# Performance work log

Measured on AMD Instinct MI355X. Metric: run time of the kernel, lower is better.

Reference implementation:

```python
import jax, jax.numpy as jnp
import numpy as np

N_COMPANY = 16384
N_SECTOR = 64
PER_SECTOR = N_COMPANY // N_SECTOR  # 256, companies grouped contiguously by sector
WIN = 32
D_IN = 16
H_GRU = 64
H_INTRA = 64
H_INTER = 64
D_OUT = 4
E_INNER = 524288  # avg degree 32 within sectors


def setup_inputs() -> dict:
    key = jax.random.key(0)
    ks = jax.random.split(key, 20)
    s = 0.05

    daily_data_batch = jax.random.normal(ks[0], (WIN, N_COMPANY, D_IN), jnp.float32)

    rng = np.random.default_rng(0)
    dst = rng.integers(0, N_COMPANY, E_INNER)
    src = (dst // PER_SECTOR) * PER_SECTOR + rng.integers(0, PER_SECTOR, E_INNER)  # same-sector neighbors
    inner_edge = jnp.asarray(np.stack([src, dst]), jnp.int32)

    a, b = np.meshgrid(np.arange(N_SECTOR), np.arange(N_SECTOR), indexing="ij")
    oe = np.stack([a.ravel(), b.ravel()])
    oe = oe[:, oe[0] != oe[1]]  # fully-connected sector graph w/o self loops (GAT adds them)
    outer_edge = jnp.asarray(oe, jnp.int32)

    sector_ids = jnp.asarray(np.arange(N_COMPANY) // PER_SECTOR, jnp.int32)

    inp = {
        "daily_data_batch": daily_data_batch,
        "inner_edge": inner_edge,
        "outer_edge": outer_edge,
        "sector_ids": sector_ids,
        # BatchNorm1d(input_dim*window_size)
        "bn_gamma": jnp.ones((D_IN * WIN,), jnp.float32),
        "bn_beta": jnp.zeros((D_IN * WIN,), jnp.float32),
        # Graph GRU (per-node learnable initial hidden state)
        "gru_Wih": s * jax.random.normal(ks[1], (D_IN, 3 * H_GRU), jnp.float32),
        "gru_Whh": s * jax.random.normal(ks[2], (H_GRU, 3 * H_GRU), jnp.float32),
        "gru_bih": jnp.zeros((3 * H_GRU,), jnp.float32),
        "gru_bhh": jnp.zeros((3 * H_GRU,), jnp.float32),
        "gru_h0": s * jax.random.normal(ks[3], (N_COMPANY, H_GRU), jnp.float32),
        # intra-sector GATConv
        "gat1_W": s * jax.random.normal(ks[4], (H_GRU, H_INTRA), jnp.float32),
        "gat1_asrc": s * jax.random.normal(ks[5], (H_INTRA,), jnp.float32),
        "gat1_adst": s * jax.random.normal(ks[6], (H_INTRA,), jnp.float32),
        "gat1_b": jnp.zeros((H_INTRA,), jnp.float32),
        # inter-sector GATConv
        "gat2_W": s * jax.random.normal(ks[7], (H_INTRA, H_INTER), jnp.float32),
        "gat2_asrc": s * jax.random.normal(ks[8], (H_INTER,), jnp.float32),
        "gat2_adst": s * jax.random.normal(ks[9], (H_INTER,), jnp.float32),
        "gat2_b": jnp.zeros((H_INTER,), jnp.float32),
        # fusion / logit heads
        "fusion_W": s * jax.random.normal(ks[10], (H_GRU + H_INTRA + H_INTER, H_GRU), jnp.float32),
        "fusion_b": jnp.zeros((H_GRU,), jnp.float32),
        "logit_W": s * jax.random.normal(ks[11], (H_GRU, D_OUT), jnp.float32),
        "logit_b": jnp.zeros((D_OUT,), jnp.float32),
    }
    return inp


def _gat(x, edge, W, a_src, a_dst, b):
    """PyG-style single-head GATConv with default add_self_loops=True."""
    N = x.shape[0]
    h = x @ W  # [N, F]
    loops = jnp.arange(N, dtype=edge.dtype)
    src = jnp.concatenate([edge[0], loops])
    dst = jnp.concatenate([edge[1], loops])
    e = jax.nn.leaky_relu(h[src] @ a_src + h[dst] @ a_dst, 0.2)  # [E]
    # segment softmax over incoming edges per dst node
    m = jax.ops.segment_max(e, dst, num_segments=N)
    ex = jnp.exp(e - m[dst])
    denom = jax.ops.segment_sum(ex, dst, num_segments=N)
    alpha = ex / (denom[dst] + 1e-16)
    out = jax.ops.segment_sum(h[src] * alpha[:, None], dst, num_segments=N)
    return out + b


def _forward(daily_data_batch, inner_edge, outer_edge, sector_ids,
             bn_gamma, bn_beta,
             gru_Wih, gru_Whh, gru_bih, gru_bhh, gru_h0,
             gat1_W, gat1_asrc, gat1_adst, gat1_b,
             gat2_W, gat2_asrc, gat2_adst, gat2_b,
             fusion_W, fusion_b, logit_W, logit_b):
    W, N, D = daily_data_batch.shape
    # BatchNorm1d over companies (train-mode batch stats, eps=1e-5)
    xb = jnp.transpose(daily_data_batch, (1, 0, 2)).reshape(N, W * D)
    mu = xb.mean(axis=0)
    var = xb.var(axis=0)
    xb = (xb - mu) * jax.lax.rsqrt(var + 1e-5) * bn_gamma + bn_beta
    x = jnp.transpose(xb.reshape(N, W, D), (1, 0, 2))  # [W, N, D]

    # GRU over the window, per-node hidden state
    def step(h, xt):
        gi = xt @ gru_Wih + gru_bih
        gh = h @ gru_Whh + gru_bhh
        ir, iz, inn = jnp.split(gi, 3, axis=-1)
        hr, hz, hn = jnp.split(gh, 3, axis=-1)
        r = jax.nn.sigmoid(ir + hr)
        z = jax.nn.sigmoid(iz + hz)
        n = jnp.tanh(inn + r * hn)
        return (1.0 - z) * n + z * h, None

    seq_emb, _ = jax.lax.scan(step, gru_h0, x)  # [N, H_GRU]

    intra_emb = _gat(seq_emb, inner_edge, gat1_W, gat1_asrc, gat1_adst, gat1_b)  # [N, H_INTRA]

    # sector_separater + per-sector max pooling == segment_max
    sec_pool = jax.ops.segment_max(intra_emb, sector_ids, num_segments=N_SECTOR)  # [S, H_INTRA]
    sec_emb = _gat(sec_pool, outer_edge, gat2_W, gat2_asrc, gat2_adst, gat2_b)  # [S, H_INTER]
    sec_broad = sec_emb[sector_ids]  # repeat_interleave back to companies

    fusion_vec = jnp.concatenate([seq_emb, sec_broad, intra_emb], axis=-1)
    fusion_vec = jax.nn.relu(fusion_vec @ fusion_W + fusion_b)
    logits = jax.nn.softmax(fusion_vec @ logit_W + logit_b, axis=1)
    logits = jnp.cumsum(logits, axis=1)
    eps = 5e-08
    return jnp.clip(logits, eps, 1.0 - eps)


def reference(daily_data_batch, inner_edge, outer_edge, sector_ids,
              bn_gamma, bn_beta,
              gru_Wih, gru_Whh, gru_bih, gru_bhh, gru_h0,
              gat1_W, gat1_asrc, gat1_adst, gat1_b,
              gat2_W, gat2_asrc, gat2_adst, gat2_b,
              fusion_W, fusion_b, logit_W, logit_b):
    return _forward(daily_data_batch, inner_edge, outer_edge, sector_ids,
                    bn_gamma, bn_beta,
                    gru_Wih, gru_Whh, gru_bih, gru_bhh, gru_h0,
                    gat1_W, gat1_asrc, gat1_adst, gat1_b,
                    gat2_W, gat2_asrc, gat2_adst, gat2_b,
                    fusion_W, fusion_b, logit_W, logit_b)
```

## Files before the change

### kernel.cpp

```cpp
#include <hip/hip_runtime.h>

#define NC 16384
#define WIN 32
#define DI 16
#define EI 524288

typedef unsigned short u16;
typedef unsigned char u8;
typedef unsigned int u32;
typedef __attribute__((ext_vector_type(8))) short bfrag8;
typedef __attribute__((ext_vector_type(4))) float facc4;

__device__ __forceinline__ float bf2f(u16 u) { return __uint_as_float(((u32)u) << 16); }
__device__ __forceinline__ u16 f2bf(float f) {
    u32 u = __float_as_uint(f);
    u += 0x7FFFu + ((u >> 16) & 1u);
    return (u16)(u >> 16);
}
__device__ __forceinline__ float frcp(float x) { return __builtin_amdgcn_rcpf(x); }
__device__ __forceinline__ float lrelu(float x) { return x >= 0.0f ? x : 0.2f * x; }
__device__ __forceinline__ float loadf(const void* p, size_t i, bool f32) {
    return f32 ? ((const float*)p)[i] : bf2f(((const u16*)p)[i]);
}
__device__ __forceinline__ bool is_f32(const void* gamma) {
    return ((const u32*)gamma)[0] == 0x3F800000u;
}

#define O_SCALE 0
#define O_SHIFT 512
#define O_WIH   1024
#define O_WHH   4096
#define O_BIH   16384
#define O_BHH   16576
#define O_G1W   16768
#define O_G1AS  20864
#define O_G1AD  20928
#define O_G1B   20992
#define O_G2W   21056
#define O_G2AS  25152
#define O_G2AD  25216
#define O_G2B   25280
#define O_FB    25344
#define O_LW    25408
#define O_LB    25664
#define O_FW16  25668
#define O_BNACC 31812
#define O_SEQ   40960
#define O_H1    1089536
#define O_INTRA 1613824
#define O_SPOOL 2138112
#define O_AS    2158592
#define O_AD    2174976
#define O_M     2191360

__global__ __launch_bounds__(256) void k_convert(const void* __restrict__ gamma,
                                                 const void* __restrict__ wih,
                                                 const void* __restrict__ whh,
                                                 const void* __restrict__ bih,
                                                 const void* __restrict__ bhh,
                                                 const void* __restrict__ g1w,
                                                 const void* __restrict__ g1as,
                                                 const void* __restrict__ g1ad,
                                                 const void* __restrict__ g1b,
                                                 const void* __restrict__ g2w,
                                                 const void* __restrict__ g2as,
                                                 const void* __restrict__ g2ad,
                                                 const void* __restrict__ g2b,
                                                 const void* __restrict__ fw,
                                                 const void* __restrict__ fb,
                                                 const void* __restrict__ lw,
                                                 const void* __restrict__ lb,
                                                 float* __restrict__ ws,
                                                 uint4* __restrict__ M16) {
    int gt = blockIdx.x * 256 + threadIdx.x;
    const int GS = 64 * 256;
    bool f32 = is_f32(gamma);
    u16* fw16 = (u16*)(ws + O_FW16);
    for (int i = gt; i < 3072; i += GS) ws[O_WIH + i] = loadf(wih, i, f32);
    for (int i = gt; i < 12288; i += GS) {
        ws[O_WHH + i] = loadf(whh, i, f32);
        fw16[i] = f32 ? f2bf(((const float*)fw)[i]) : ((const u16*)fw)[i];
    }
    for (int i = gt; i < 192; i += GS) {
        ws[O_BIH + i] = loadf(bih, i, f32);
        ws[O_BHH + i] = loadf(bhh, i, f32);
    }
    for (int i = gt; i < 4096; i += GS) {
        ws[O_G1W + i] = loadf(g1w, i, f32);
        ws[O_G2W + i] = loadf(g2w, i, f32);
    }
    if (gt < 64) {
        ws[O_G1AS + gt] = loadf(g1as, gt, f32);
        ws[O_G1AD + gt] = loadf(g1ad, gt, f32);
        ws[O_G1B + gt] = loadf(g1b, gt, f32);
        ws[O_G2AS + gt] = loadf(g2as, gt, f32);
        ws[O_G2AD + gt] = loadf(g2ad, gt, f32);
        ws[O_G2B + gt] = loadf(g2b, gt, f32);
        ws[O_FB + gt] = loadf(fb, gt, f32);
    }
    if (gt < 256) ws[O_LW + gt] = loadf(lw, gt, f32);
    if (gt < 4) ws[O_LB + gt] = loadf(lb, gt, f32);
    for (int i = gt; i < 1024; i += GS) ws[O_BNACC + i] = 0.f;
    const uint4 z4 = {0u, 0u, 0u, 0u};
    for (int i = gt; i < 262144; i += GS) M16[i] = z4;
}

__global__ __launch_bounds__(256) void k_prep(const void* __restrict__ daily,
                                              const void* __restrict__ gamma,
                                              float* __restrict__ bnacc,
                                              const int* __restrict__ edges,
                                              u32* __restrict__ M32) {
    __shared__ float rS[256 * 17];
    __shared__ float rQ[256 * 17];
    int bid = blockIdx.x;
    int tid = threadIdx.x;
    if (bid >= 128) {
        int g = (bid - 128) * 256 + tid;
        int4 s4 = ((const int4*)edges)[g];
        int4 d4 = ((const int4*)(edges + EI))[g];
        int ss[4] = {s4.x, s4.y, s4.z, s4.w};
        int dd[4] = {d4.x, d4.y, d4.z, d4.w};
#pragma unroll
        for (int i = 0; i < 4; i++) {
            int sl = ss[i] & 255;
            atomicAdd(&M32[dd[i] * 64 + (sl >> 2)], 1u << ((sl & 3) * 8));
        }
        return;
    }
    int w = bid >> 2, ch = bid & 3;
    bool f32 = is_f32(gamma);
    float s[16], q[16];
#pragma unroll
    for (int i = 0; i < 16; i++) { s[i] = 0.f; q[i] = 0.f; }
    for (int it = 0; it < 16; it++) {
        int c = ch * 4096 + it * 256 + tid;
        size_t base = ((size_t)w * NC + c) * DI;
        float v[16];
        if (f32) {
            const float4* p = (const float4*)((const float*)daily + base);
            float4 a = p[0], b = p[1], cc = p[2], d = p[3];
            v[0] = a.x; v[1] = a.y; v[2] = a.z; v[3] = a.w;
            v[4] = b.x; v[5] = b.y; v[6] = b.z; v[7] = b.w;
            v[8] = cc.x; v[9] = cc.y; v[10] = cc.z; v[11] = cc.w;
            v[12] = d.x; v[13] = d.y; v[14] = d.z; v[15] = d.w;
        } else {
            const uint4* p = (const uint4*)((const u16*)daily + base);
            uint4 a = p[0], b = p[1];
            u32 us[8] = {a.x, a.y, a.z, a.w, b.x, b.y, b.z, b.w};
#pragma unroll
            for (int i = 0; i < 8; i++) {
                v[2 * i] = __uint_as_float(us[i] << 16);
                v[2 * i + 1] = __uint_as_float(us[i] & 0xFFFF0000u);
            }
        }
#pragma unroll
        for (int i = 0; i < 16; i++) { s[i] += v[i]; q[i] += v[i] * v[i]; }
    }
#pragma unroll
    for (int i = 0; i < 16; i++) { rS[tid * 17 + i] = s[i]; rQ[tid * 17 + i] = q[i]; }
    __syncthreads();
    int f = tid & 15, g = tid >> 4;
    float ss = 0.f, qq = 0.f;
    for (int t = g * 16; t < g * 16 + 16; t++) { ss += rS[t * 17 + f]; qq += rQ[t * 17 + f]; }
    atomicAdd(&bnacc[w * 16 + f], ss);
    atomicAdd(&bnacc[512 + w * 16 + f], qq);
}

__global__ __launch_bounds__(256, 4) void k_gru(const void* __restrict__ daily,
                                                const void* __restrict__ gamma,
                                                const void* __restrict__ beta,
                                                const void* __restrict__ h0_g,
                                                const float* __restrict__ ws,
                                                float* __restrict__ seq_out,
                                                u16* __restrict__ h1_out,
                                                float* __restrict__ asg,
                                                float* __restrict__ adg) {
    __shared__ __attribute__((aligned(16))) u16 sHd[2][16 * 72];
    __shared__ float sSc[512], sSh[512];
    __shared__ float sRed[2][4][16];
    int tid = threadIdx.x;
    int w = tid >> 6, lane = tid & 63;
    int li = lane & 15, q = lane >> 4;
    int col = w * 16 + li;
    int n0 = blockIdx.x * 16;
    bool f32 = is_f32(gamma);

    for (int f = tid; f < 512; f += 256) {
        float mu = ws[O_BNACC + f] * (1.0f / NC);
        float var = ws[O_BNACC + 512 + f] * (1.0f / NC) - mu * mu;
        float sc = loadf(gamma, f, f32) * rsqrtf(var + 1e-5f);
        sSc[f] = sc;
        sSh[f] = loadf(beta, f, f32) - mu * sc;
    }

    bfrag8 bh[3][2], bx[3];
#pragma unroll
    for (int g = 0; g < 3; g++) {
        float sc = (g < 2) ? -1.0f : -2.0f;
#pragma unroll
        for (int kc = 0; kc < 2; kc++)
#pragma unroll
            for (int j = 0; j < 8; j++) {
                int k = kc * 32 + q * 8 + j;
                bh[g][kc][j] = (short)f2bf(sc * ws[O_WHH + k * 192 + g * 64 + col]);
            }
#pragma unroll
        for (int j = 0; j < 8; j++) {
            int k = q * 8 + j;
            bx[g][j] = (k < 16) ? (short)f2bf(sc * ws[O_WIH + k * 192 + g * 64 + col]) : (short)0;
        }
    }
    float bR = -1.0f * (ws[O_BIH + col] + ws[O_BHH + col]);
    float bZ = -1.0f * (ws[O_BIH + 64 + col] + ws[O_BHH + 64 + col]);
    float bNX = -2.0f * ws[O_BIH + 128 + col];
    float bNH = -2.0f * ws[O_BHH + 128 + col];

    float hC[4];
#pragma unroll
    for (int r = 0; r < 4; r++)
        hC[r] = loadf(h0_g, (size_t)(n0 + q * 4 + r) * 64 + col, f32);
    if (tid < 128) {
        int hr = tid >> 3, hc = (tid & 7) * 8;
        u16 hrow[8];
#pragma unroll
        for (int i = 0; i < 8; i++)
            hrow[i] = f2bf(loadf(h0_g, (size_t)(n0 + hr) * 64 + hc + i, f32));
        *(uint4*)&sHd[0][hr * 72 + hc] = *(const uint4*)&hrow[0];
    }
    __syncthreads();

    bool xl = (q < 2);
    float xr[8];
    if (xl) {
        size_t base = ((size_t)(n0 + li)) * DI + q * 8;
        if (f32) {
            float4 a = *(const float4*)((const float*)daily + base);
            float4 b = *(const float4*)((const float*)daily + base + 4);
            xr[0] = a.x; xr[1] = a.y; xr[2] = a.z; xr[3] = a.w;
            xr[4] = b.x; xr[5] = b.y; xr[6] = b.z; xr[7] = b.w;
        } else {
            ushort4 a = *(const ushort4*)((const u16*)daily + base);
            ushort4 b = *(const ushort4*)((const u16*)daily + base + 4);
            xr[0] = bf2f(a.x); xr[1] = bf2f(a.y); xr[2] = bf2f(a.z); xr[3] = bf2f(a.w);
            xr[4] = bf2f(b.x); xr[5] = bf2f(b.y); xr[6] = bf2f(b.z); xr[7] = bf2f(b.w);
        }
    }

    for (int t = 0; t < WIN; t++) {
        int p = t & 1;
        bfrag8 ax = (bfrag8){0, 0, 0, 0, 0, 0, 0, 0};
        if (xl) {
            int sb = t * 16 + q * 8;
#pragma unroll
            for (int j = 0; j < 8; j++)
                ax[j] = (short)f2bf(xr[j] * sSc[sb + j] + sSh[sb + j]);
        }
        bfrag8 ah0 = *(const bfrag8*)&sHd[p][li * 72 + q * 8];
        bfrag8 ah1 = *(const bfrag8*)&sHd[p][li * 72 + 32 + q * 8];
        if (xl && t < WIN - 1) {
            size_t base = ((size_t)(t + 1) * NC + n0 + li) * DI + q * 8;
            if (f32) {
                float4 a = *(const float4*)((const float*)daily + base);
                float4 b = *(const float4*)((const float*)daily + base + 4);
                xr[0] = a.x; xr[1] = a.y; xr[2] = a.z; xr[3] = a.w;
                xr[4] = b.x; xr[5] = b.y; xr[6] = b.z; xr[7] = b.w;
            } else {
                ushort4 a = *(const ushort4*)((const u16*)daily + base);
                ushort4 b = *(const ushort4*)((const u16*)daily + base + 4);
                xr[0] = bf2f(a.x); xr[1] = bf2f(a.y); xr[2] = bf2f(a.z); xr[3] = bf2f(a.w);
                xr[4] = bf2f(b.x); xr[5] = bf2f(b.y); xr[6] = bf2f(b.z); xr[7] = bf2f(b.w);
            }
        }
        facc4 aR = __builtin_amdgcn_mfma_f32_16x16x32_bf16(ah0, bh[0][0], (facc4){bR, bR, bR, bR}, 0, 0, 0);
        facc4 aZ = __builtin_amdgcn_mfma_f32_16x16x32_bf16(ah0, bh[1][0], (facc4){bZ, bZ, bZ, bZ}, 0, 0, 0);
        facc4 aNH = __builtin_amdgcn_mfma_f32_16x16x32_bf16(ah0, bh[2][0], (facc4){bNH, bNH, bNH, bNH}, 0, 0, 0);
        facc4 aNX = __builtin_amdgcn_mfma_f32_16x16x32_bf16(ax, bx[2], (facc4){bNX, bNX, bNX, bNX}, 0, 0, 0);
        aR = __builtin_amdgcn_mfma_f32_16x16x32_bf16(ah1, bh[0][1], aR, 0, 0, 0);
        aZ = __builtin_amdgcn_mfma_f32_16x16x32_bf16(ah1, bh[1][1], aZ, 0, 0, 0);
        aNH = __builtin_amdgcn_mfma_f32_16x16x32_bf16(ah1, bh[2][1], aNH, 0, 0, 0);
        aR = __builtin_amdgcn_mfma_f32_16x16x32_bf16(ax, bx[0], aR, 0, 0, 0);
        aZ = __builtin_amdgcn_mfma_f32_16x16x32_bf16(ax, bx[1], aZ, 0, 0, 0);
#pragma unroll
        for (int r = 0; r < 4; r++) {
            float gr = frcp(1.0f + __expf(aR[r]));
            float gz = frcp(1.0f + __expf(aZ[r]));
            float narg = aNX[r] + gr * aNH[r];
            float gn = 2.0f * frcp(1.0f + __expf(narg)) - 1.0f;
            hC[r] = gn + gz * (hC[r] - gn);
        }
#pragma unroll
        for (int r = 0; r < 4; r++)
            sHd[p ^ 1][(q * 4 + r) * 72 + col] = f2bf(hC[r]);
        __syncthreads();
    }

#pragma unroll
    for (int r = 0; r < 4; r++)
        seq_out[(size_t)(n0 + q * 4 + r) * 64 + col] = hC[r];

    const facc4 zf = {0.f, 0.f, 0.f, 0.f};
    bfrag8 a0 = *(const bfrag8*)&sHd[0][li * 72 + q * 8];
    bfrag8 a1 = *(const bfrag8*)&sHd[0][li * 72 + 32 + q * 8];
    bfrag8 bg0, bg1;
#pragma unroll
    for (int j = 0; j < 8; j++) {
        bg0[j] = (short)f2bf(ws[O_G1W + (q * 8 + j) * 64 + col]);
        bg1[j] = (short)f2bf(ws[O_G1W + (32 + q * 8 + j) * 64 + col]);
    }
    facc4 acc = __builtin_amdgcn_mfma_f32_16x16x32_bf16(a0, bg0, zf, 0, 0, 0);
    acc = __builtin_amdgcn_mfma_f32_16x16x32_bf16(a1, bg1, acc, 0, 0, 0);
    float a1s_j = ws[O_G1AS + col], a1d_j = ws[O_G1AD + col];
    float pAs[4], pAd[4];
#pragma unroll
    for (int r = 0; r < 4; r++) {
        h1_out[(size_t)(n0 + q * 4 + r) * 64 + col] = f2bf(acc[r]);
        pAs[r] = acc[r] * a1s_j;
        pAd[r] = acc[r] * a1d_j;
    }
#pragma unroll
    for (int o = 1; o < 16; o <<= 1) {
#pragma unroll
        for (int r = 0; r < 4; r++) {
            pAs[r] += __shfl_xor(pAs[r], o);
            pAd[r] += __shfl_xor(pAd[r], o);
        }
    }
    if (li == 0) {
#pragma unroll
        for (int r = 0; r < 4; r++) {
            sRed[0][w][q * 4 + r] = pAs[r];
            sRed[1][w][q * 4 + r] = pAd[r];
        }
    }
    __syncthreads();
    if (tid < 16) {
        asg[n0 + tid] = sRed[0][0][tid] + sRed[0][1][tid] + sRed[0][2][tid] + sRed[0][3][tid];
        adg[n0 + tid] = sRed[1][0][tid] + sRed[1][1][tid] + sRed[1][2][tid] + sRed[1][3][tid];
    }
}

__global__ __launch_bounds__(256) void k_gat1agg(const u16* __restrict__ h1g,
                                                 const float* __restrict__ ws,
                                                 const u8* __restrict__ M8,
                                                 const float* __restrict__ asg,
                                                 const float* __restrict__ adg,
                                                 u16* __restrict__ intra,
                                                 float* __restrict__ spool4) {
    __shared__ __attribute__((aligned(16))) u16 hT[64 * 264];
    __shared__ __attribute__((aligned(16))) u16 sP[64 * 136];
    __shared__ float sAs[256], sAd[64], sB[64], sRS[64];
    __shared__ float sRSp[4][64];
    __shared__ float wmax[4];
    int tid = threadIdx.x;
    int sector = blockIdx.x >> 2;
    int dstbase = sector * 256 + (blockIdx.x & 3) * 64;
    int sbase = sector * 256;
    {
        const u16* row = h1g + (size_t)(sbase + tid) * 64;
#pragma unroll
        for (int c = 0; c < 16; c++) {
            uint2 v = ((const uint2*)row)[c];
            hT[(c * 4 + 0) * 264 + tid] = (u16)(v.x & 0xffff);
            hT[(c * 4 + 1) * 264 + tid] = (u16)(v.x >> 16);
            hT[(c * 4 + 2) * 264 + tid] = (u16)(v.y & 0xffff);
            hT[(c * 4 + 3) * 264 + tid] = (u16)(v.y >> 16);
        }
    }
    sAs[tid] = asg[sbase + tid];
    if (tid < 64) { sAd[tid] = adg[dstbase + tid]; sB[tid] = ws[O_G1B + tid]; }
    __syncthreads();
    int lane = tid & 63, w = tid >> 6;
    int li = lane & 15, q = lane >> 4;
    {
        float a = sAs[tid];
#pragma unroll
        for (int o = 1; o < 64; o <<= 1) a = fmaxf(a, __shfl_xor(a, o));
        if (lane == 0) wmax[w] = a;
    }
    __syncthreads();
    float maxA = fmaxf(fmaxf(wmax[0], wmax[1]), fmaxf(wmax[2], wmax[3]));

    int prow = tid >> 2, pcg = tid & 3;
    float adr_p = sAd[prow];
    float mrow_p = lrelu(maxA + adr_p);
    float lsum = 0.f;

    facc4 acc[4];
#pragma unroll
    for (int mt = 0; mt < 4; mt++) acc[mt] = (facc4){0.f, 0.f, 0.f, 0.f};

#pragma unroll
    for (int half = 0; half < 2; half++) {
        const u8* mp = M8 + (size_t)(dstbase + prow) * 256 + half * 128 + pcg * 32;
        uint4 mva = *(const uint4*)mp;
        uint4 mvb = *(const uint4*)(mp + 16);
        u32 wsrc[8] = {mva.x, mva.y, mva.z, mva.w, mvb.x, mvb.y, mvb.z, mvb.w};
#pragma unroll
        for (int i2 = 0; i2 < 16; i2++) {
            int i0 = 2 * i2;
            u32 mb0 = (wsrc[i0 >> 2] >> ((i0 & 3) * 8)) & 255u;
            u32 mb1 = (wsrc[i0 >> 2] >> (((i0 + 1) & 3) * 8)) & 255u;
            int c = half * 128 + pcg * 32 + i0;
            float e0 = lrelu(sAs[c] + adr_p);
            float e1 = lrelu(sAs[c + 1] + adr_p);
            float v0 = (float)mb0 * __expf(e0 - mrow_p);
            float v1 = (float)mb1 * __expf(e1 - mrow_p);
            u16 b0 = f2bf(v0), b1 = f2bf(v1);
            *(u32*)&sP[prow * 136 + pcg * 32 + i0] = (u32)b0 | ((u32)b1 << 16);
            lsum += bf2f(b0) + bf2f(b1);
        }
        __syncthreads();
#pragma unroll
        for (int kc = 0; kc < 4; kc++) {
            bfrag8 bfh = *(const bfrag8*)&hT[(w * 16 + li) * 264 + half * 128 + kc * 32 + q * 8];
#pragma unroll
            for (int mt = 0; mt < 4; mt++) {
                bfrag8 af = *(const bfrag8*)&sP[(mt * 16 + li) * 136 + kc * 32 + q * 8];
                acc[mt] = __builtin_amdgcn_mfma_f32_16x16x32_bf16(af, bfh, acc[mt], 0, 0, 0);
            }
        }
        __syncthreads();
    }
    sRSp[pcg][prow] = lsum;
    __syncthreads();
    if (tid < 64) sRS[tid] = sRSp[0][tid] + sRSp[1][tid] + sRSp[2][tid] + sRSp[3][tid];
    __syncthreads();

    float vmax = -1e30f;
    int colL = w * 16 + li;
#pragma unroll
    for (int mt = 0; mt < 4; mt++) {
#pragma unroll
        for (int r = 0; r < 4; r++) {
            int row = mt * 16 + q * 4 + r;
            int d = dstbase + row;
            int selfI = (blockIdx.x & 3) * 64 + row;
            float adr = sAd[row];
            float es = lrelu(sAs[selfI] + adr);
            float mrow = lrelu(maxA + adr);
            float exS = __expf(es - mrow);
            float denom = sRS[row] + exS;
            float inv = frcp(denom + 1e-16f);
            float selfh = bf2f(hT[colL * 264 + selfI]);
            float val = (acc[mt][r] + exS * selfh) * inv + sB[colL];
            intra[(size_t)d * 64 + colL] = f2bf(val);
            vmax = fmaxf(vmax, val);
        }
    }
    vmax = fmaxf(vmax, __shfl_xor(vmax, 16));
    vmax = fmaxf(vmax, __shfl_xor(vmax, 32));
    if (q == 0) spool4[(size_t)blockIdx.x * 64 + colL] = vmax;
}

__global__ __launch_bounds__(256) void k_fusion(const float* __restrict__ seq,
                                                const float* __restrict__ spool4,
                                                const u16* __restrict__ intra,
                                                const float* __restrict__ ws,
                                                const void* __restrict__ gamma,
                                                void* __restrict__ out) {
    __shared__ __attribute__((aligned(16))) union {
        struct { float sPt[4096]; float sW2[4096]; float sH2[4096]; } p0;
        struct { u16 sV[64 * 200]; float sFus[64 * 68]; } p1;
    } U;
    __shared__ float sSemb[64], sAs2[64], sAd2[64];
    __shared__ float sFB[64], sLW[256], sLB[4];
    __shared__ float red2[512];
    int tid = threadIdx.x, n0 = blockIdx.x * 64;
    int sid = blockIdx.x >> 2;
    bool f32 = is_f32(gamma);

    for (int i = tid; i < 4096; i += 256) {
        int n = i >> 6, k = i & 63;
        float m = fmaxf(fmaxf(spool4[(n * 4 + 0) * 64 + k], spool4[(n * 4 + 1) * 64 + k]),
                        fmaxf(spool4[(n * 4 + 2) * 64 + k], spool4[(n * 4 + 3) * 64 + k]));
        U.p0.sPt[k * 64 + n] = m;
        U.p0.sW2[i] = ws[O_G2W + i];
    }
    __syncthreads();
    {
        int n = tid >> 2, jg = tid & 3, j0 = jg * 16;
        float acc0[16];
#pragma unroll
        for (int i = 0; i < 16; i++) acc0[i] = 0.f;
        for (int k = 0; k < 64; k++) {
            float a = U.p0.sPt[k * 64 + n];
#pragma unroll
            for (int i = 0; i < 16; i += 4) {
                float4 w4 = *(const float4*)&U.p0.sW2[k * 64 + j0 + i];
                acc0[i] += a * w4.x; acc0[i + 1] += a * w4.y; acc0[i + 2] += a * w4.z; acc0[i + 3] += a * w4.w;
            }
        }
#pragma unroll
        for (int i = 0; i < 16; i++) U.p0.sH2[n * 64 + j0 + i] = acc0[i];
        float ps = 0.f, pd = 0.f;
#pragma unroll
        for (int i = 0; i < 16; i++) { ps += acc0[i] * ws[O_G2AS + j0 + i]; pd += acc0[i] * ws[O_G2AD + j0 + i]; }
        red2[(n * 4 + jg) * 2] = ps;
        red2[(n * 4 + jg) * 2 + 1] = pd;
    }
    __syncthreads();
    if (tid < 64) {
        float s = 0.f, dd = 0.f;
        for (int g = 0; g < 4; g++) { s += red2[(tid * 4 + g) * 2]; dd += red2[(tid * 4 + g) * 2 + 1]; }
        sAs2[tid] = s; sAd2[tid] = dd;
    }
    __syncthreads();
    if (tid < 64) {
        float e = lrelu(sAs2[tid] + sAd2[sid]);
        float m = e;
        for (int o = 32; o; o >>= 1) m = fmaxf(m, __shfl_xor(m, o));
        float ex = __expf(e - m);
        float den = ex;
        for (int o = 32; o; o >>= 1) den += __shfl_xor(den, o);
        float inv = frcp(den + 1e-16f);
        float o_ = 0.f;
        for (int l = 0; l < 64; l++) {
            float a = __shfl(ex, l);
            o_ += a * U.p0.sH2[l * 64 + tid];
        }
        sSemb[tid] = o_ * inv + ws[O_G2B + tid];
    }
    if (tid < 64) sFB[tid] = ws[O_FB + tid];
    sLW[tid] = ws[O_LW + tid];
    if (tid < 4) sLB[tid] = ws[O_LB + tid];
    __syncthreads();

    {
        int c = tid >> 2, p = tid & 3;
        u16 px[16];
        const float* rp = seq + (size_t)(n0 + c) * 64 + p * 16;
#pragma unroll
        for (int i = 0; i < 16; i += 4) {
            float4 v = *(const float4*)&rp[i];
            px[i] = f2bf(v.x); px[i + 1] = f2bf(v.y); px[i + 2] = f2bf(v.z); px[i + 3] = f2bf(v.w);
        }
        *(uint4*)&U.p1.sV[c * 200 + p * 16] = *(const uint4*)&px[0];
        *(uint4*)&U.p1.sV[c * 200 + p * 16 + 8] = *(const uint4*)&px[8];
#pragma unroll
        for (int i = 0; i < 16; i++) px[i] = f2bf(sSemb[p * 16 + i]);
        *(uint4*)&U.p1.sV[c * 200 + 64 + p * 16] = *(const uint4*)&px[0];
        *(uint4*)&U.p1.sV[c * 200 + 64 + p * 16 + 8] = *(const uint4*)&px[8];
        const u16* ip = intra + (size_t)(n0 + c) * 64 + p * 16;
        *(uint4*)&U.p1.sV[c * 200 + 128 + p * 16] = *(const uint4*)ip;
        *(uint4*)&U.p1.sV[c * 200 + 128 + p * 16 + 8] = *(const uint4*)(ip + 8);
    }
    int lane = tid & 63, w = tid >> 6;
    int li = lane & 15, q = lane >> 4;
    int colw = w * 16 + li;
    const u16* fw16g = (const u16*)(ws + O_FW16);
    bfrag8 bwf[6];
#pragma unroll
    for (int kc = 0; kc < 6; kc++)
#pragma unroll
        for (int j = 0; j < 8; j++)
            bwf[kc][j] = (short)fw16g[(kc * 32 + q * 8 + j) * 64 + colw];
    __syncthreads();

    facc4 acc[4];
#pragma unroll
    for (int mt = 0; mt < 4; mt++) acc[mt] = (facc4){0.f, 0.f, 0.f, 0.f};
#pragma unroll
    for (int kc = 0; kc < 6; kc++) {
#pragma unroll
        for (int mt = 0; mt < 4; mt++) {
            bfrag8 av = *(const bfrag8*)&U.p1.sV[(mt * 16 + li) * 200 + kc * 32 + q * 8];
            acc[mt] = __builtin_amdgcn_mfma_f32_16x16x32_bf16(av, bwf[kc], acc[mt], 0, 0, 0);
        }
    }
    float fb = sFB[colw];
#pragma unroll
    for (int mt = 0; mt < 4; mt++)
#pragma unroll
        for (int r = 0; r < 4; r++) {
            float v = fmaxf(acc[mt][r] + fb, 0.f);
            U.p1.sFus[(mt * 16 + q * 4 + r) * 68 + colw] = v;
        }
    __syncthreads();

    if (tid < 64) {
        float l[4] = {sLB[0], sLB[1], sLB[2], sLB[3]};
        for (int j = 0; j < 64; j++) {
            float v = U.p1.sFus[tid * 68 + j];
            l[0] += v * sLW[j * 4 + 0];
            l[1] += v * sLW[j * 4 + 1];
            l[2] += v * sLW[j * 4 + 2];
            l[3] += v * sLW[j * 4 + 3];
        }
        float m = fmaxf(fmaxf(l[0], l[1]), fmaxf(l[2], l[3]));
        float e0 = __expf(l[0] - m), e1 = __expf(l[1] - m), e2 = __expf(l[2] - m), e3 = __expf(l[3] - m);
        float is = frcp(e0 + e1 + e2 + e3);
        float c0 = e0 * is;
        float c1 = c0 + e1 * is;
        float c2 = c1 + e2 * is;
        float c3 = c2 + e3 * is;
        const float lo = 5e-8f, hi = 1.0f - 5e-8f;
        c0 = fminf(fmaxf(c0, lo), hi);
        c1 = fminf(fmaxf(c1, lo), hi);
        c2 = fminf(fmaxf(c2, lo), hi);
        c3 = fminf(fmaxf(c3, lo), hi);
        size_t ob = (size_t)(n0 + tid) * 4;
        if (f32) {
            *(float4*)&((float*)out)[ob] = make_float4(c0, c1, c2, c3);
        } else {
            *(ushort4*)&((u16*)out)[ob] = make_ushort4(f2bf(c0), f2bf(c1), f2bf(c2), f2bf(c3));
        }
    }
}

extern "C" void kernel_launch(void* const* d_in, const int* in_sizes, int n_in,
                              void* d_out, int out_size, void* d_ws, size_t ws_size,
                              hipStream_t stream) {
    const void* daily = d_in[0];
    const int* inner = (const int*)d_in[1];
    const void* gamma = d_in[4];
    const void* beta = d_in[5];
    const void* wih = d_in[6];
    const void* whh = d_in[7];
    const void* bih = d_in[8];
    const void* bhh = d_in[9];
    const void* h0 = d_in[10];
    const void* g1w = d_in[11];
    const void* g1as = d_in[12];
    const void* g1ad = d_in[13];
    const void* g1b = d_in[14];
    const void* g2w = d_in[15];
    const void* g2as = d_in[16];
    const void* g2ad = d_in[17];
    const void* g2b = d_in[18];
    const void* fw = d_in[19];
    const void* fb = d_in[20];
    const void* lw = d_in[21];
    const void* lb = d_in[22];

    float* ws = (float*)d_ws;
    u16* h1g = (u16*)(ws + O_H1);
    u16* intra = (u16*)(ws + O_INTRA);
    u8* M8 = (u8*)(ws + O_M);

    k_convert<<<64, 256, 0, stream>>>(gamma, wih, whh, bih, bhh, g1w, g1as, g1ad, g1b,
                                      g2w, g2as, g2ad, g2b, fw, fb, lw, lb, ws, (uint4*)M8);
    k_prep<<<640, 256, 0, stream>>>(daily, gamma, ws + O_BNACC, inner, (u32*)M8);
    k_gru<<<1024, 256, 0, stream>>>(daily, gamma, beta, h0, ws, ws + O_SEQ, h1g, ws + O_AS, ws + O_AD);
    k_gat1agg<<<256, 256, 0, stream>>>(h1g, ws, M8, ws + O_AS, ws + O_AD, intra, ws + O_SPOOL);
    k_fusion<<<256, 256, 0, stream>>>(ws + O_SEQ, ws + O_SPOOL, intra, ws, gamma, d_out);
}
```

Baseline: 226.7 us.

## Preload and normalize all GRU inputs into LDS; split prep kernels, memset adjacency

The GRU kernel now loads the whole 32-step input window for its 16 nodes up front, applies batch-norm, converts to bf16 and stores it in shared memory. The recurrent loop then reads each step's fragment from LDS instead of issuing per-step global loads and conversions. The fused prep kernel is split into separate BN-statistics and edge-histogram kernels, and the adjacency zeroing moves from a kernel loop to hipMemsetAsync. This adds about 24KB of LDS per block, which may lower occupancy, and adds extra launches.

```diff
diff --git a/kernel.cpp b/kernel.cpp
--- a/kernel.cpp
+++ b/kernel.cpp
@@ -70,8 +70,7 @@
                                                  const void* __restrict__ fb,
                                                  const void* __restrict__ lw,
                                                  const void* __restrict__ lb,
-                                                 float* __restrict__ ws,
-                                                 uint4* __restrict__ M16) {
+                                                 float* __restrict__ ws) {
     int gt = blockIdx.x * 256 + threadIdx.x;
     const int GS = 64 * 256;
     bool f32 = is_f32(gamma);
@@ -101,33 +100,15 @@
     if (gt < 256) ws[O_LW + gt] = loadf(lw, gt, f32);
     if (gt < 4) ws[O_LB + gt] = loadf(lb, gt, f32);
     for (int i = gt; i < 1024; i += GS) ws[O_BNACC + i] = 0.f;
-    const uint4 z4 = {0u, 0u, 0u, 0u};
-    for (int i = gt; i < 262144; i += GS) M16[i] = z4;
-}
-
-__global__ __launch_bounds__(256) void k_prep(const void* __restrict__ daily,
-                                              const void* __restrict__ gamma,
-                                              float* __restrict__ bnacc,
-                                              const int* __restrict__ edges,
-                                              u32* __restrict__ M32) {
+}
+
+__global__ __launch_bounds__(256) void k_bnpart(const void* __restrict__ daily,
+                                                const void* __restrict__ gamma,
+                                                float* __restrict__ bnacc) {
     __shared__ float rS[256 * 17];
     __shared__ float rQ[256 * 17];
-    int bid = blockIdx.x;
+    int w = blockIdx.x >> 2, ch = blockIdx.x & 3;
     int tid = threadIdx.x;
-    if (bid >= 128) {
-        int g = (bid - 128) * 256 + tid;
-        int4 s4 = ((const int4*)edges)[g];
-        int4 d4 = ((const int4*)(edges + EI))[g];
-        int ss[4] = {s4.x, s4.y, s4.z, s4.w};
-        int dd[4] = {d4.x, d4.y, d4.z, d4.w};
-#pragma unroll
-        for (int i = 0; i < 4; i++) {
-            int sl = ss[i] & 255;
-            atomicAdd(&M32[dd[i] * 64 + (sl >> 2)], 1u << ((sl & 3) * 8));
-        }
-        return;
-    }
-    int w = bid >> 2, ch = bid & 3;
     bool f32 = is_f32(gamma);
     float s[16], q[16];
 #pragma unroll
@@ -166,6 +147,19 @@
     atomicAdd(&bnacc[512 + w * 16 + f], qq);
 }
 
+__global__ __launch_bounds__(256) void k_edge(const int* __restrict__ edges, u32* __restrict__ M32) {
+    int g = blockIdx.x * 256 + threadIdx.x;
+    int4 s4 = ((const int4*)edges)[g];
+    int4 d4 = ((const int4*)(edges + EI))[g];
+    int ss[4] = {s4.x, s4.y, s4.z, s4.w};
+    int dd[4] = {d4.x, d4.y, d4.z, d4.w};
+#pragma unroll
+    for (int i = 0; i < 4; i++) {
+        int sl = ss[i] & 255;
+        atomicAdd(&M32[dd[i] * 64 + (sl >> 2)], 1u << ((sl & 3) * 8));
+    }
+}
+
 __global__ __launch_bounds__(256, 4) void k_gru(const void* __restrict__ daily,
                                                 const void* __restrict__ gamma,
                                                 const void* __restrict__ beta,
@@ -176,6 +170,7 @@
                                                 float* __restrict__ asg,
                                                 float* __restrict__ adg) {
     __shared__ __attribute__((aligned(16))) u16 sHd[2][16 * 72];
+    __shared__ __attribute__((aligned(16))) u16 sXall[512 * 24];
     __shared__ float sSc[512], sSh[512];
     __shared__ float sRed[2][4][16];
     int tid = threadIdx.x;
@@ -192,6 +187,34 @@
         sSc[f] = sc;
         sSh[f] = loadf(beta, f, f32) - mu * sc;
     }
+    __syncthreads();
+    for (int R = tid; R < 512; R += 256) {
+        int t = R >> 4, m = R & 15;
+        size_t base = ((size_t)t * NC + n0 + m) * DI;
+        float xv[16];
+        if (f32) {
+            const float4* p = (const float4*)((const float*)daily + base);
+            float4 a = p[0], b = p[1], c = p[2], d = p[3];
+            xv[0] = a.x; xv[1] = a.y; xv[2] = a.z; xv[3] = a.w;
+            xv[4] = b.x; xv[5] = b.y; xv[6] = b.z; xv[7] = b.w;
+            xv[8] = c.x; xv[9] = c.y; xv[10] = c.z; xv[11] = c.w;
+            xv[12] = d.x; xv[13] = d.y; xv[14] = d.z; xv[15] = d.w;
+        } else {
+            const uint4* p = (const uint4*)((const u16*)daily + base);
+            uint4 a = p[0], b = p[1];
+            u32 us[8] = {a.x, a.y, a.z, a.w, b.x, b.y, b.z, b.w};
+#pragma unroll
+            for (int i = 0; i < 8; i++) {
+                xv[2 * i] = __uint_as_float(us[i] << 16);
+                xv[2 * i + 1] = __uint_as_float(us[i] & 0xFFFF0000u);
+            }
+        }
+        u16 px[16];
+#pragma unroll
+        for (int i = 0; i < 16; i++) px[i] = f2bf(xv[i] * sSc[t * 16 + i] + sSh[t * 16 + i]);
+        *(uint4*)&sXall[R * 24] = *(const uint4*)&px[0];
+        *(uint4*)&sXall[R * 24 + 8] = *(const uint4*)&px[8];
+    }
 
     bfrag8 bh[3][2], bx[3];
 #pragma unroll
@@ -230,47 +253,12 @@
     __syncthreads();
 
     bool xl = (q < 2);
-    float xr[8];
-    if (xl) {
-        size_t base = ((size_t)(n0 + li)) * DI + q * 8;
-        if (f32) {
-            float4 a = *(const float4*)((const float*)daily + base);
-            float4 b = *(const float4*)((const float*)daily + base + 4);
-            xr[0] = a.x; xr[1] = a.y; xr[2] = a.z; xr[3] = a.w;
-            xr[4] = b.x; xr[5] = b.y; xr[6] = b.z; xr[7] = b.w;
-        } else {
-            ushort4 a = *(const ushort4*)((const u16*)daily + base);
-            ushort4 b = *(const ushort4*)((const u16*)daily + base + 4);
-            xr[0] = bf2f(a.x); xr[1] = bf2f(a.y); xr[2] = bf2f(a.z); xr[3] = bf2f(a.w);
-            xr[4] = bf2f(b.x); xr[5] = bf2f(b.y); xr[6] = bf2f(b.z); xr[7] = bf2f(b.w);
-        }
-    }
-
     for (int t = 0; t < WIN; t++) {
         int p = t & 1;
         bfrag8 ax = (bfrag8){0, 0, 0, 0, 0, 0, 0, 0};
-        if (xl) {
-            int sb = t * 16 + q * 8;
-#pragma unroll
-            for (int j = 0; j < 8; j++)
-                ax[j] = (short)f2bf(xr[j] * sSc[sb + j] + sSh[sb + j]);
-        }
+        if (xl) ax = *(const bfrag8*)&sXall[(t * 16 + li) * 24 + q * 8];
         bfrag8 ah0 = *(const bfrag8*)&sHd[p][li * 72 + q * 8];
         bfrag8 ah1 = *(const bfrag8*)&sHd[p][li * 72 + 32 + q * 8];
-        if (xl && t < WIN - 1) {
-            size_t base = ((size_t)(t + 1) * NC + n0 + li) * DI + q * 8;
-            if (f32) {
-                float4 a = *(const float4*)((const float*)daily + base);
-                float4 b = *(const float4*)((const float*)daily + base + 4);
-                xr[0] = a.x; xr[1] = a.y; xr[2] = a.z; xr[3] = a.w;
-                xr[4] = b.x; xr[5] = b.y; xr[6] = b.z; xr[7] = b.w;
-            } else {
-                ushort4 a = *(const ushort4*)((const u16*)daily + base);
-                ushort4 b = *(const ushort4*)((const u16*)daily + base + 4);
-                xr[0] = bf2f(a.x); xr[1] = bf2f(a.y); xr[2] = bf2f(a.z); xr[3] = bf2f(a.w);
-                xr[4] = bf2f(b.x); xr[5] = bf2f(b.y); xr[6] = bf2f(b.z); xr[7] = bf2f(b.w);
-            }
-        }
         facc4 aR = __builtin_amdgcn_mfma_f32_16x16x32_bf16(ah0, bh[0][0], (facc4){bR, bR, bR, bR}, 0, 0, 0);
         facc4 aZ = __builtin_amdgcn_mfma_f32_16x16x32_bf16(ah0, bh[1][0], (facc4){bZ, bZ, bZ, bZ}, 0, 0, 0);
         facc4 aNH = __builtin_amdgcn_mfma_f32_16x16x32_bf16(ah0, bh[2][0], (facc4){bNH, bNH, bNH, bNH}, 0, 0, 0);
@@ -637,9 +625,11 @@
     u16* intra = (u16*)(ws + O_INTRA);
     u8* M8 = (u8*)(ws + O_M);
 
+    hipMemsetAsync((void*)M8, 0, (size_t)NC * 256, stream);
     k_convert<<<64, 256, 0, stream>>>(gamma, wih, whh, bih, bhh, g1w, g1as, g1ad, g1b,
-                                      g2w, g2as, g2ad, g2b, fw, fb, lw, lb, ws, (uint4*)M8);
-    k_prep<<<640, 256, 0, stream>>>(daily, gamma, ws + O_BNACC, inner, (u32*)M8);
+                                      g2w, g2as, g2ad, g2b, fw, fb, lw, lb, ws);
+    k_bnpart<<<128, 256, 0, stream>>>(daily, gamma, ws + O_BNACC);
+    k_edge<<<512, 256, 0, stream>>>(inner, (u32*)M8);
     k_gru<<<1024, 256, 0, stream>>>(daily, gamma, beta, h0, ws, ws + O_SEQ, h1g, ws + O_AS, ws + O_AD);
     k_gat1agg<<<256, 256, 0, stream>>>(h1g, ws, M8, ws + O_AS, ws + O_AD, intra, ws + O_SPOOL);
     k_fusion<<<256, 256, 0, stream>>>(ws + O_SEQ, ws + O_SPOOL, intra, ws, gamma, d_out);
```

New measurement: 228.9 us. About the same (+1.0%).
